# Kernel tuning notes

Hardware: AMD Instinct MI355X
Metric: run time of the kernel (lower is better)

## Reference

```python
import jax, jax.numpy as jnp
import numpy as np

B = 256          # graphs per batch
NR = 268         # ROIs (nodes) per graph
N = B * NR       # total nodes
IC, OC = 256, 64 # in/out channels
NC = 7           # communities
DEG = 32
E = N * DEG      # total edges
K = int(NR * 0.8)  # 214 nodes kept per graph (floor, as torch .long())
LN_EPS = 1e-5


def setup_inputs() -> dict:
    key = jax.random.key(0)
    ks = jax.random.split(key, 10)
    x = jax.random.normal(ks[0], (N, IC), jnp.float32)
    # within-graph random edges: local src/dst in [0, NR) plus per-graph offset
    src = jax.random.randint(ks[1], (E,), 0, NR, dtype=jnp.int32)
    dst = jax.random.randint(ks[2], (E,), 0, NR, dtype=jnp.int32)
    off = jnp.repeat(jnp.arange(B, dtype=jnp.int32) * NR, NR * DEG)
    edge_index = jnp.stack([src + off, dst + off])  # (2, E)
    edge_attr = jax.random.uniform(ks[3], (E, 1), jnp.float32)
    batch = jnp.repeat(jnp.arange(B, dtype=jnp.int32), NR)
    xav = lambda k, shp: jax.random.normal(k, shp, jnp.float32) * np.float32(
        np.sqrt(2.0 / (shp[-2] + shp[-1])))
    return {
        "x": x, "edge_index": edge_index, "edge_attr": edge_attr, "batch": batch,
        "basis_kernels": xav(ks[4], (NC, IC, OC)),
        "roi_community": xav(ks[5], (NR, NC)),
        "ew_w": xav(ks[6], (1, OC)), "ew_b": jnp.zeros((OC,), jnp.float32),
        "conv_bias": jnp.zeros((OC,), jnp.float32),
        "ln_gamma": jnp.ones((OC,), jnp.float32), "ln_beta": jnp.zeros((OC,), jnp.float32),
        "att_w1": xav(ks[7], (OC, OC)), "att_b1": jnp.zeros((OC,), jnp.float32),
        "att_w2": xav(ks[8], (OC, 1)), "att_b2": jnp.zeros((1,), jnp.float32),
    }


def reference(x, edge_index, edge_attr, batch, basis_kernels, roi_community,
              ew_w, ew_b, conv_bias, ln_gamma, ln_beta,
              att_w1, att_b1, att_w2, att_b2):
    n = x.shape[0]
    loops = jnp.arange(n, dtype=edge_index.dtype)
    ei = jnp.concatenate([edge_index, jnp.stack([loops, loops])], axis=1)  # add self loops
    ea = jnp.concatenate([edge_attr, jnp.ones((n, 1), x.dtype)], axis=0)   # fill_value=1.0

    # ROI-aware kernels: per-node mixture of basis kernels
    cw = jax.nn.softmax(roi_community, axis=-1)            # (NR, NC)
    roi_k = jnp.einsum('rc,cio->rio', cw, basis_kernels)   # (NR, IC, OC)
    node_ids = loops % NR
    node_k = roi_k[node_ids]                               # (N, IC, OC) gather
    xt = jnp.einsum('ni,nio->no', x, node_k)               # per-node bmm

    # edge-gated message passing, scatter-add aggregation
    gate = jax.nn.sigmoid(ea @ ew_w + ew_b)                # (E+N, OC)
    msg = xt[ei[0]] * gate
    out = jax.ops.segment_sum(msg, ei[1], num_segments=n) + conv_bias

    out = jax.nn.elu(out)
    mu = jnp.mean(out, axis=-1, keepdims=True)
    var = jnp.mean(jnp.square(out - mu), axis=-1, keepdims=True)
    h = (out - mu) * jax.lax.rsqrt(var + LN_EPS) * ln_gamma + ln_beta
    # dropout: eval mode (identity)

    # R-pool: per-graph top-k (all graphs have NR contiguous nodes)
    scores = (jnp.tanh(h @ att_w1 + att_b1) @ att_w2 + att_b2).squeeze(-1)  # (N,)
    top_v, top_i = jax.lax.top_k(scores.reshape(B, NR), K)                  # (B, K)
    perm = (top_i.astype(jnp.int32) + jnp.arange(B, dtype=jnp.int32)[:, None] * NR).reshape(-1)
    x_pooled = h[perm] * jax.nn.sigmoid(top_v.reshape(-1))[:, None]
    batch_pooled = batch[perm]
    return x_pooled, batch_pooled, scores, perm
```

## Files before the change

kernel.cpp:

```cpp
#include <hip/hip_runtime.h>
#include <cstdint>
#include <cstddef>

#define NR   268
#define NB   256
#define NN   (NR*NB)
#define IC   256
#define OC   64
#define DEG  32
#define EPG  (NR*DEG)
#define NE   (NN*DEG)
#define KK   214

#define XP_OFF 0
#define BP_OFF 3506176
#define SC_OFF 3560960
#define PM_OFF 3629568

#define WS_ROIK 0
#define WS_XT   4390912
#define WS_META 8781824
#define WS_ROWS 13369344

#define PPG   4480
#define ZROW  (NR*OC)

typedef float v2f __attribute__((ext_vector_type(2)));

__device__ __forceinline__ v2f pkfma(v2f a, v2f b, v2f c) {
    v2f d;
    asm("v_pk_fma_f32 %0, %1, %2, %3" : "=v"(d) : "v"(a), "v"(b), "v"(c));
    return d;
}

__global__ __launch_bounds__(256) void k_roik(const float* __restrict__ rc,
                                              const float* __restrict__ basis,
                                              float* __restrict__ roik) {
    int r = blockIdx.x;
    float c[7];
    float m = -1e30f;
#pragma unroll
    for (int j = 0; j < 7; ++j) { c[j] = rc[r*7 + j]; m = fmaxf(m, c[j]); }
    float s = 0.f;
#pragma unroll
    for (int j = 0; j < 7; ++j) { c[j] = expf(c[j] - m); s += c[j]; }
    float inv = 1.f / s;
#pragma unroll
    for (int j = 0; j < 7; ++j) c[j] *= inv;
    for (int idx = threadIdx.x; idx < IC*OC; idx += 256) {
        float acc = 0.f;
#pragma unroll
        for (int j = 0; j < 7; ++j) acc = fmaf(c[j], basis[j*IC*OC + idx], acc);
        roik[(size_t)r*IC*OC + idx] = acc;
    }
}

#define GS3 130
__global__ __launch_bounds__(512) void k_xtf(const float* __restrict__ x,
                                             const float* __restrict__ roik,
                                             float* __restrict__ xt) {
    __shared__ float sXT[32 * GS3];

    int bid = blockIdx.x;
    int r = bid % NR;
    int half = bid / NR;
    int tid = threadIdx.x;
    int lane = tid & 63;
    int wu = __builtin_amdgcn_readfirstlane(tid >> 6);
    int g0 = lane * 2;
    int o0 = wu * 8;

    const float* __restrict__ wk = roik + (size_t)r * (IC*OC);

    int quad = tid & 7, grp = tid >> 3;
    const float* __restrict__ xrowA =
        x + ((size_t)(half*128 + grp) * NR + r) * IC + quad*4;
    const float* __restrict__ xrowB = xrowA + (size_t)64 * NR * IC;

    float acc[2][8];
#pragma unroll
    for (int i = 0; i < 2; ++i)
#pragma unroll
        for (int j = 0; j < 8; ++j) acc[i][j] = 0.f;

    for (int kt = 0; kt < IC; kt += 32) {
        __syncthreads();
        {
            float4 xa = *(const float4*)(xrowA + kt);
            float4 xb = *(const float4*)(xrowB + kt);
            sXT[(quad*4+0)*GS3 + grp] = xa.x;
            sXT[(quad*4+1)*GS3 + grp] = xa.y;
            sXT[(quad*4+2)*GS3 + grp] = xa.z;
            sXT[(quad*4+3)*GS3 + grp] = xa.w;
            sXT[(quad*4+0)*GS3 + 64 + grp] = xb.x;
            sXT[(quad*4+1)*GS3 + 64 + grp] = xb.y;
            sXT[(quad*4+2)*GS3 + 64 + grp] = xb.z;
            sXT[(quad*4+3)*GS3 + 64 + grp] = xb.w;
        }
        __syncthreads();

#pragma unroll 8
        for (int k = 0; k < 32; ++k) {
            float2 xa = *(const float2*)&sXT[k*GS3 + g0];
            const float* wrow = wk + (size_t)(kt + k) * OC + o0;
#pragma unroll
            for (int j = 0; j < 8; ++j) {
                float wv = wrow[j];
                acc[0][j] = fmaf(xa.x, wv, acc[0][j]);
                acc[1][j] = fmaf(xa.y, wv, acc[1][j]);
            }
        }
    }

#pragma unroll
    for (int i = 0; i < 2; ++i) {
        int g = half*128 + g0 + i;
        float* p = xt + ((size_t)g * NR + r) * OC + o0;
        float4 a; a.x = acc[i][0]; a.y = acc[i][1]; a.z = acc[i][2]; a.w = acc[i][3];
        float4 b; b.x = acc[i][4]; b.y = acc[i][5]; b.z = acc[i][6]; b.w = acc[i][7];
        *(float4*)p = a;
        *(float4*)(p + 4) = b;
    }
}

#define NREP2 16
__global__ __launch_bounds__(1024) void k_csr(const int* __restrict__ ei,
                                              const float* __restrict__ ea,
                                              float* __restrict__ meta,
                                              unsigned int* __restrict__ rows) {
    int g = blockIdx.x;
    __shared__ unsigned int cnt[NREP2][NR];
    __shared__ unsigned int cur[NREP2][NR];
    __shared__ unsigned int tot[NR];
    __shared__ unsigned int prs[NR];
    int tid = threadIdx.x;
    int wid = tid >> 6;
    for (int i = tid; i < NREP2*NR; i += 1024) ((unsigned*)cnt)[i] = 0u;
    __syncthreads();
    int ebase = g * EPG;
    for (int e = tid; e < EPG; e += 1024) {
        int ld = ei[NE + ebase + e] - g * NR;
        atomicAdd(&cnt[wid][ld], 1u);
    }
    __syncthreads();
    for (int r = tid; r < NR; r += 1024) {
        unsigned t = 0;
#pragma unroll
        for (int s = 0; s < NREP2; ++s) t += cnt[s][r];
        tot[r] = t;
    }
    __syncthreads();
    if (tid < 64) {
        unsigned run = 0;
        for (int base = 0; base < NR; base += 64) {
            int idx = base + tid;
            unsigned v = (idx < NR) ? ((tot[idx] + 1u) >> 1) : 0u;
            unsigned orig = v;
#pragma unroll
            for (int s = 1; s < 64; s <<= 1) {
                int t = __shfl_up((int)v, (unsigned)s, 64);
                if (tid >= s) v += (unsigned)t;
            }
            if (idx < NR) prs[idx] = run + v - orig;
            run += (unsigned)__shfl((int)v, 63, 64);
        }
    }
    __syncthreads();
    for (int r = tid; r < NR; r += 1024) {
        unsigned base = 0;
#pragma unroll
        for (int s = 0; s < NREP2; ++s) { cur[s][r] = base; base += cnt[s][r]; }
    }
    __syncthreads();
    unsigned lastPairs = (tot[NR-1] + 1u) >> 1;
    for (int i = tid; i < NR + 1; i += 1024)
        rows[(size_t)g * (NR + 1) + i] =
            (i < NR) ? prs[i] : (prs[NR-1] + lastPairs);
    float* mg = meta + (size_t)g * PPG * 4;
    for (int e = tid; e < EPG; e += 1024) {
        int src = ei[ebase + e];
        int ld  = ei[NE + ebase + e] - g * NR;
        float a = ea[ebase + e];
        unsigned rank = atomicAdd(&cur[wid][ld], 1u);
        unsigned p = prs[ld] + (rank >> 1), sl = rank & 1u;
        mg[(size_t)p*4 + sl]     = __int_as_float((src - g*NR) * OC);
        mg[(size_t)p*4 + 2 + sl] = a - 0.5f;
    }
    __syncthreads();
    for (int r = tid; r < NR; r += 1024) {
        if (tot[r] & 1u) {
            unsigned p = prs[r] + (tot[r] >> 1);
            mg[(size_t)p*4 + 1] = __int_as_float(ZROW);
            mg[(size_t)p*4 + 3] = 0.f;
        }
    }
}

__global__ __launch_bounds__(1024, 4) void k_fused(
    const float* __restrict__ xt,
    const float4* __restrict__ meta,
    const unsigned int* __restrict__ rows,
    const float* __restrict__ ew_w, const float* __restrict__ ew_b,
    const float* __restrict__ conv_bias,
    const float* __restrict__ ln_g, const float* __restrict__ ln_b,
    const float* __restrict__ w1, const float* __restrict__ b1,
    const float* __restrict__ w2, const float* __restrict__ b2,
    float* __restrict__ out)
{
    extern __shared__ float smem[];
    float* xts = smem;
    float* hls = smem + (NR*OC + 64);
    __shared__ float rowbuf[16][OC];
    __shared__ float scl[NR];
    __shared__ int ord[KK];

    int g = blockIdx.x;
    int tid = threadIdx.x;
    int o = tid & 63, w = tid >> 6;

    {
        const float4* s4 = (const float4*)(xt + (size_t)g * NR * OC);
        float4* d4 = (float4*)xts;
        for (int i = tid; i < NR*OC/4; i += 1024) d4[i] = s4[i];
        if (tid < 16) d4[NR*OC/4 + tid] = make_float4(0.f, 0.f, 0.f, 0.f);
    }

    float wo = ew_w[o], bo = ew_b[o], cb = conv_bias[o];
    float lng = ln_g[o], lnb = ln_b[o];
    float w2o = w2[o], b1o = b1[o], b2s = b2[0];
    float sgself = 1.f / (1.f + expf(-(wo + bo)));

    float z0 = fmaf(0.5f, wo, bo);
    float sg0 = 1.f / (1.f + expf(-z0));
    float u  = sg0 * (1.f - sg0);
    float d2 = u * (1.f - 2.f*sg0);
    float d3 = u * (1.f - 6.f*u);
    float d4c = d2 * (1.f - 12.f*u);
    float k1 = u * wo;
    float k2 = d2 * wo*wo * 0.5f;
    float k3 = d3 * wo*wo*wo * (1.f/6.f);
    float k4 = d4c * wo*wo*wo*wo * (1.f/24.f);
    v2f kd4 = {k4, k4}, kd3 = {k3, k3}, kd2 = {k2, k2}, kd1 = {k1, k1};
    v2f sdv = {sg0, sg0};

    #define LOADW(j) \
        v2f wcA##j = { w1[(4*j+0)*OC+o], w1[(4*j+1)*OC+o] }; \
        v2f wcB##j = { w1[(4*j+2)*OC+o], w1[(4*j+3)*OC+o] };
    LOADW(0)  LOADW(1)  LOADW(2)  LOADW(3)
    LOADW(4)  LOADW(5)  LOADW(6)  LOADW(7)
    LOADW(8)  LOADW(9)  LOADW(10) LOADW(11)
    LOADW(12) LOADW(13) LOADW(14) LOADW(15)
    #undef LOADW

    const float4* __restrict__ gm = meta + (size_t)g * PPG;
    const unsigned int* __restrict__ gr = rows + (size_t)g * (NR + 1);
    const float* __restrict__ xo = xts + o;
    __syncthreads();

    #define PAIR(mp, acc) { \
        v2f xv; \
        xv.x = xo[__float_as_int((mp).x)]; \
        xv.y = xo[__float_as_int((mp).y)]; \
        v2f dv = { (mp).z, (mp).w }; \
        v2f t = pkfma(kd4, dv, kd3); \
        t = pkfma(t, dv, kd2); \
        t = pkfma(t, dv, kd1); \
        t = pkfma(t, dv, sdv); \
        acc = pkfma(xv, t, acc); }

    for (int r = w; r < NR; r += 16) {
        unsigned js = __builtin_amdgcn_readfirstlane(gr[r]);
        unsigned je = __builtin_amdgcn_readfirstlane(gr[r + 1]);
        v2f acc; acc.x = xts[r*OC + o] * sgself; acc.y = 0.f;
        unsigned j = js;
        for (; j + 8 <= je; j += 8) {
            float4 m0 = gm[j],   m1 = gm[j+1], m2 = gm[j+2], m3 = gm[j+3];
            float4 m4 = gm[j+4], m5 = gm[j+5], m6 = gm[j+6], m7 = gm[j+7];
            PAIR(m0, acc) PAIR(m1, acc) PAIR(m2, acc) PAIR(m3, acc)
            PAIR(m4, acc) PAIR(m5, acc) PAIR(m6, acc) PAIR(m7, acc)
        }
        if (j + 4 <= je) {
            float4 m0 = gm[j], m1 = gm[j+1], m2 = gm[j+2], m3 = gm[j+3];
            PAIR(m0, acc) PAIR(m1, acc) PAIR(m2, acc) PAIR(m3, acc)
            j += 4;
        }
        for (; j < je; ++j) {
            float4 m0 = gm[j];
            PAIR(m0, acc)
        }
        float accs = acc.x + acc.y + cb;
        float v = accs > 0.f ? accs : expm1f(accs);
        float s1 = v;
#pragma unroll
        for (int m = 1; m < 64; m <<= 1) s1 += __shfl_xor(s1, m, 64);
        float mu = s1 * (1.f/64.f);
        float d = v - mu;
        float s2 = d * d;
#pragma unroll
        for (int m = 1; m < 64; m <<= 1) s2 += __shfl_xor(s2, m, 64);
        float rsd = rsqrtf(s2 * (1.f/64.f) + 1e-5f);
        float h = fmaf(d * rsd, lng, lnb);
        hls[r*OC + o] = h;
        rowbuf[w][o] = h;
        {
            const float* hr = rowbuf[w];
            v2f tA = { b1o, 0.f }, tB = { 0.f, 0.f };
            #define STEP(j) { float4 h4 = *(const float4*)(hr + 4*j); \
                v2f hl = { h4.x, h4.y }, hh = { h4.z, h4.w }; \
                tA = pkfma(hl, wcA##j, tA); tB = pkfma(hh, wcB##j, tB); }
            STEP(0)  STEP(1)  STEP(2)  STEP(3)
            STEP(4)  STEP(5)  STEP(6)  STEP(7)
            STEP(8)  STEP(9)  STEP(10) STEP(11)
            STEP(12) STEP(13) STEP(14) STEP(15)
            #undef STEP
            float t = (tA.x + tA.y) + (tB.x + tB.y);
            float a2 = fminf(fmaxf(2.f * t, -80.f), 80.f);
            float y = expf(a2);
            float th = (y - 1.f) / (y + 1.f);
            float p = th * w2o;
#pragma unroll
            for (int m = 1; m < 64; m <<= 1) p += __shfl_xor(p, m, 64);
            if (o == 0) {
                float sc = p + b2s;
                scl[r] = sc;
                out[SC_OFF + (size_t)g * NR + r] = sc;
            }
        }
    }
    #undef PAIR
    __syncthreads();

    if (tid < NR) {
        float sr = scl[tid];
        int rank = 0;
        for (int jj = 0; jj < NR; ++jj) {
            float sj = scl[jj];
            rank += (sj > sr) || (sj == sr && jj < tid);
        }
        if (rank < KK) ord[rank] = tid;
    }
    __syncthreads();

    for (int k = w; k < KK; k += 16) {
        int r = ord[k];
        float v = scl[r];
        float gate = 1.f / (1.f + expf(-v));
        float hvv = hls[r*OC + o];
        out[XP_OFF + ((size_t)g*KK + k)*64 + o] = hvv * gate;
        if (o == 0) {
            out[BP_OFF + (size_t)g*KK + k] = (float)g;
            out[PM_OFF + (size_t)g*KK + k] = (float)(g*NR + r);
        }
    }
}

extern "C" void kernel_launch(void* const* d_in, const int* in_sizes, int n_in,
                              void* d_out, int out_size, void* d_ws, size_t ws_size,
                              hipStream_t stream) {
    const float* x     = (const float*)d_in[0];
    const int*   ei    = (const int*)d_in[1];
    const float* ea    = (const float*)d_in[2];
    const float* basis = (const float*)d_in[4];
    const float* rc    = (const float*)d_in[5];
    const float* ew_w  = (const float*)d_in[6];
    const float* ew_b  = (const float*)d_in[7];
    const float* cbias = (const float*)d_in[8];
    const float* ln_g  = (const float*)d_in[9];
    const float* ln_b  = (const float*)d_in[10];
    const float* w1    = (const float*)d_in[11];
    const float* b1    = (const float*)d_in[12];
    const float* w2    = (const float*)d_in[13];
    const float* b2    = (const float*)d_in[14];
    float* out = (float*)d_out;

    float* wsf = (float*)d_ws;
    float* roik = wsf + WS_ROIK;
    float* xtb  = wsf + WS_XT;
    float* metaF = wsf + WS_META;
    unsigned int* rows = (unsigned int*)(wsf + WS_ROWS);

    size_t fused_lds = (size_t)(NR*OC + 64 + NR*OC) * sizeof(float);

    k_roik <<<dim3(NR),   dim3(256), 0, stream>>>(rc, basis, roik);
    k_xtf  <<<dim3(NR*2), dim3(512), 0, stream>>>(x, roik, xtb);
    k_csr  <<<dim3(NB),   dim3(1024), 0, stream>>>(ei, ea, metaF, rows);
    k_fused<<<dim3(NB),   dim3(1024), fused_lds, stream>>>(
                                                  xtb, (const float4*)metaF, rows,
                                                  ew_w, ew_b, cbias, ln_g, ln_b,
                                                  w1, b1, w2, b2, out);
}
```

Before: 320.1 us.

## Merge ROI-kernel and CSR prep kernels, use DPP wave reductions, drop rowbuf

Result: slower. 379.2 us (+18.4%).

```diff
diff --git a/kernel.cpp b/kernel.cpp
--- a/kernel.cpp
+++ b/kernel.cpp
@@ -33,25 +33,117 @@
     return d;
 }
 
-__global__ __launch_bounds__(256) void k_roik(const float* __restrict__ rc,
-                                              const float* __restrict__ basis,
-                                              float* __restrict__ roik) {
-    int r = blockIdx.x;
-    float c[7];
-    float m = -1e30f;
-#pragma unroll
-    for (int j = 0; j < 7; ++j) { c[j] = rc[r*7 + j]; m = fmaxf(m, c[j]); }
-    float s = 0.f;
-#pragma unroll
-    for (int j = 0; j < 7; ++j) { c[j] = expf(c[j] - m); s += c[j]; }
-    float inv = 1.f / s;
-#pragma unroll
-    for (int j = 0; j < 7; ++j) c[j] *= inv;
-    for (int idx = threadIdx.x; idx < IC*OC; idx += 256) {
-        float acc = 0.f;
-#pragma unroll
-        for (int j = 0; j < 7; ++j) acc = fmaf(c[j], basis[j*IC*OC + idx], acc);
-        roik[(size_t)r*IC*OC + idx] = acc;
+template<int CTRL>
+__device__ __forceinline__ float dppadd(float x) {
+    int s = __builtin_amdgcn_update_dpp(0, __float_as_int(x), CTRL, 0xf, 0xf, true);
+    return x + __int_as_float(s);
+}
+__device__ __forceinline__ float wave_sum64(float v) {
+    v = dppadd<0xB1>(v);
+    v = dppadd<0x4E>(v);
+    v = dppadd<0x141>(v);
+    v = dppadd<0x140>(v);
+    v += __shfl_xor(v, 16, 64);
+    v += __shfl_xor(v, 32, 64);
+    return v;
+}
+
+#define NREP2 16
+__global__ __launch_bounds__(1024) void k_prep(const float* __restrict__ rc,
+                                               const float* __restrict__ basis,
+                                               float* __restrict__ roik,
+                                               const int* __restrict__ ei,
+                                               const float* __restrict__ ea,
+                                               float* __restrict__ meta,
+                                               unsigned int* __restrict__ rows) {
+    __shared__ unsigned int cnt[NREP2][NR];
+    __shared__ unsigned int cur[NREP2][NR];
+    __shared__ unsigned int tot[NR];
+    __shared__ unsigned int prs[NR];
+    int b = blockIdx.x;
+    int tid = threadIdx.x;
+
+    if (b >= NB) {
+        int r = b - NB;
+        float c[7];
+        float m = -1e30f;
+#pragma unroll
+        for (int j = 0; j < 7; ++j) { c[j] = rc[r*7 + j]; m = fmaxf(m, c[j]); }
+        float s = 0.f;
+#pragma unroll
+        for (int j = 0; j < 7; ++j) { c[j] = expf(c[j] - m); s += c[j]; }
+        float inv = 1.f / s;
+#pragma unroll
+        for (int j = 0; j < 7; ++j) c[j] *= inv;
+        for (int idx = tid; idx < IC*OC; idx += 1024) {
+            float acc = 0.f;
+#pragma unroll
+            for (int j = 0; j < 7; ++j) acc = fmaf(c[j], basis[j*IC*OC + idx], acc);
+            roik[(size_t)r*IC*OC + idx] = acc;
+        }
+        return;
+    }
+
+    int g = b;
+    int wid = tid >> 6;
+    for (int i = tid; i < NREP2*NR; i += 1024) ((unsigned*)cnt)[i] = 0u;
+    __syncthreads();
+    int ebase = g * EPG;
+    for (int e = tid; e < EPG; e += 1024) {
+        int ld = ei[NE + ebase + e] - g * NR;
+        atomicAdd(&cnt[wid][ld], 1u);
+    }
+    __syncthreads();
+    for (int r = tid; r < NR; r += 1024) {
+        unsigned t = 0;
+#pragma unroll
+        for (int s = 0; s < NREP2; ++s) t += cnt[s][r];
+        tot[r] = t;
+    }
+    __syncthreads();
+    if (tid < 64) {
+        unsigned run = 0;
+        for (int base = 0; base < NR; base += 64) {
+            int idx = base + tid;
+            unsigned v = (idx < NR) ? ((tot[idx] + 1u) >> 1) : 0u;
+            unsigned orig = v;
+#pragma unroll
+            for (int s = 1; s < 64; s <<= 1) {
+                int t = __shfl_up((int)v, (unsigned)s, 64);
+                if (tid >= s) v += (unsigned)t;
+            }
+            if (idx < NR) prs[idx] = run + v - orig;
+            run += (unsigned)__shfl((int)v, 63, 64);
+        }
+    }
+    __syncthreads();
+    for (int r = tid; r < NR; r += 1024) {
+        unsigned base = 0;
+#pragma unroll
+        for (int s = 0; s < NREP2; ++s) { cur[s][r] = base; base += cnt[s][r]; }
+    }
+    __syncthreads();
+    unsigned lastPairs = (tot[NR-1] + 1u) >> 1;
+    for (int i = tid; i < NR + 1; i += 1024)
+        rows[(size_t)g * (NR + 1) + i] =
+            (i < NR) ? prs[i] : (prs[NR-1] + lastPairs);
+    float* mg = meta + (size_t)g * PPG * 4;
+    for (int e = tid; e < EPG; e += 1024) {
+        int src = ei[ebase + e];
+        int ld  = ei[NE + ebase + e] - g * NR;
+        float a = ea[ebase + e];
+        unsigned rank = atomicAdd(&cur[wid][ld], 1u);
+        unsigned p = prs[ld] + (rank >> 1), sl = rank & 1u;
+        mg[(size_t)p*4 + sl]     = __int_as_float((src - g*NR) * OC);
+        mg[(size_t)p*4 + 2 + sl] = a - 0.5f;
+    }
+    __syncthreads();
+    for (int r = tid; r < NR; r += 1024) {
+        if (tot[r] & 1u) {
+            unsigned p = prs[r] + (tot[r] >> 1);
+            mg[(size_t)p*4 + 1] = __int_as_float(ZROW);
+            mg[(size_t)p*4 + 3] = 0.f;
+        }
     }
 }
 
@@ -120,79 +212,6 @@
         float4 b; b.x = acc[i][4]; b.y = acc[i][5]; b.z = acc[i][6]; b.w = acc[i][7];
         *(float4*)p = a;
         *(float4*)(p + 4) = b;
-    }
-}
-
-#define NREP2 16
-__global__ __launch_bounds__(1024) void k_csr(const int* __restrict__ ei,
-                                              const float* __restrict__ ea,
-                                              float* __restrict__ meta,
-                                              unsigned int* __restrict__ rows) {
-    int g = blockIdx.x;
-    __shared__ unsigned int cnt[NREP2][NR];
-    __shared__ unsigned int cur[NREP2][NR];
-    __shared__ unsigned int tot[NR];
-    __shared__ unsigned int prs[NR];
-    int tid = threadIdx.x;
-    int wid = tid >> 6;
-    for (int i = tid; i < NREP2*NR; i += 1024) ((unsigned*)cnt)[i] = 0u;
-    __syncthreads();
-    int ebase = g * EPG;
-    for (int e = tid; e < EPG; e += 1024) {
-        int ld = ei[NE + ebase + e] - g * NR;
-        atomicAdd(&cnt[wid][ld], 1u);
-    }
-    __syncthreads();
-    for (int r = tid; r < NR; r += 1024) {
-        unsigned t = 0;
-#pragma unroll
-        for (int s = 0; s < NREP2; ++s) t += cnt[s][r];
-        tot[r] = t;
-    }
-    __syncthreads();
-    if (tid < 64) {
-        unsigned run = 0;
-        for (int base = 0; base < NR; base += 64) {
-            int idx = base + tid;
-            unsigned v = (idx < NR) ? ((tot[idx] + 1u) >> 1) : 0u;
-            unsigned orig = v;
-#pragma unroll
-            for (int s = 1; s < 64; s <<= 1) {
-                int t = __shfl_up((int)v, (unsigned)s, 64);
-                if (tid >= s) v += (unsigned)t;
-            }
-            if (idx < NR) prs[idx] = run + v - orig;
-            run += (unsigned)__shfl((int)v, 63, 64);
-        }
-    }
-    __syncthreads();
-    for (int r = tid; r < NR; r += 1024) {
-        unsigned base = 0;
-#pragma unroll
-        for (int s = 0; s < NREP2; ++s) { cur[s][r] = base; base += cnt[s][r]; }
-    }
-    __syncthreads();
-    unsigned lastPairs = (tot[NR-1] + 1u) >> 1;
-    for (int i = tid; i < NR + 1; i += 1024)
-        rows[(size_t)g * (NR + 1) + i] =
-            (i < NR) ? prs[i] : (prs[NR-1] + lastPairs);
-    float* mg = meta + (size_t)g * PPG * 4;
-    for (int e = tid; e < EPG; e += 1024) {
-        int src = ei[ebase + e];
-        int ld  = ei[NE + ebase + e] - g * NR;
-        float a = ea[ebase + e];
-        unsigned rank = atomicAdd(&cur[wid][ld], 1u);
-        unsigned p = prs[ld] + (rank >> 1), sl = rank & 1u;
-        mg[(size_t)p*4 + sl]     = __int_as_float((src - g*NR) * OC);
-        mg[(size_t)p*4 + 2 + sl] = a - 0.5f;
-    }
-    __syncthreads();
-    for (int r = tid; r < NR; r += 1024) {
-        if (tot[r] & 1u) {
-            unsigned p = prs[r] + (tot[r] >> 1);
-            mg[(size_t)p*4 + 1] = __int_as_float(ZROW);
-            mg[(size_t)p*4 + 3] = 0.f;
-        }
     }
 }
 
@@ -210,7 +229,6 @@
     extern __shared__ float smem[];
     float* xts = smem;
     float* hls = smem + (NR*OC + 64);
-    __shared__ float rowbuf[16][OC];
     __shared__ float scl[NR];
     __shared__ int ord[KK];
 
@@ -290,20 +308,15 @@
         }
         float accs = acc.x + acc.y + cb;
         float v = accs > 0.f ? accs : expm1f(accs);
-        float s1 = v;
-#pragma unroll
-        for (int m = 1; m < 64; m <<= 1) s1 += __shfl_xor(s1, m, 64);
+        float s1 = wave_sum64(v);
         float mu = s1 * (1.f/64.f);
         float d = v - mu;
-        float s2 = d * d;
-#pragma unroll
-        for (int m = 1; m < 64; m <<= 1) s2 += __shfl_xor(s2, m, 64);
+        float s2 = wave_sum64(d * d);
         float rsd = rsqrtf(s2 * (1.f/64.f) + 1e-5f);
         float h = fmaf(d * rsd, lng, lnb);
         hls[r*OC + o] = h;
-        rowbuf[w][o] = h;
         {
-            const float* hr = rowbuf[w];
+            const float* hr = hls + r*OC;
             v2f tA = { b1o, 0.f }, tB = { 0.f, 0.f };
             #define STEP(j) { float4 h4 = *(const float4*)(hr + 4*j); \
                 v2f hl = { h4.x, h4.y }, hh = { h4.z, h4.w }; \
@@ -317,9 +330,7 @@
             float a2 = fminf(fmaxf(2.f * t, -80.f), 80.f);
             float y = expf(a2);
             float th = (y - 1.f) / (y + 1.f);
-            float p = th * w2o;
-#pragma unroll
-            for (int m = 1; m < 64; m <<= 1) p += __shfl_xor(p, m, 64);
+            float p = wave_sum64(th * w2o);
             if (o == 0) {
                 float sc = p + b2s;
                 scl[r] = sc;
@@ -381,9 +392,9 @@
 
     size_t fused_lds = (size_t)(NR*OC + 64 + NR*OC) * sizeof(float);
 
-    k_roik <<<dim3(NR),   dim3(256), 0, stream>>>(rc, basis, roik);
+    k_prep <<<dim3(NB + NR), dim3(1024), 0, stream>>>(rc, basis, roik,
+                                                      ei, ea, metaF, rows);
     k_xtf  <<<dim3(NR*2), dim3(512), 0, stream>>>(x, roik, xtb);
-    k_csr  <<<dim3(NB),   dim3(1024), 0, stream>>>(ei, ea, metaF, rows);
     k_fused<<<dim3(NB),   dim3(1024), fused_lds, stream>>>(
                                                   xtb, (const float4*)metaF, rows,
                                                   ew_w, ew_b, cbias, ln_g, ln_b,
```
